# Kernel optimization log

Hardware: AMD Instinct MI355X
Metric: run time of the kernel (lower is better)

Reference implementation:

```python
import jax, jax.numpy as jnp
import numpy as np

EPS = 1e-5
K = 7            # involution kernel size
GC = 16          # group_channels (involution default)
RED = 4          # reduction ratio (involution default)


def _bn(x, g, b, m, v):
    # eval-mode BatchNorm2d over channel dim of NCHW
    scale = g / jnp.sqrt(v + EPS)
    return x * scale[None, :, None, None] + (b - m * scale)[None, :, None, None]


def setup_inputs() -> dict:
    key = jax.random.key(0)
    ks = jax.random.split(key, 24)
    C_in, C_out = 64, 128
    B, H, W = 4, 96, 96
    G = C_in // GC          # 4 involution groups
    Cr = C_in // RED        # 16 reduced channels

    def bn_params(k, c):
        k1, k2, k3, k4 = jax.random.split(k, 4)
        return (jax.random.uniform(k1, (c,)) + 0.5,          # gamma
                jax.random.normal(k2, (c,)) * 0.1,            # beta
                jax.random.normal(k3, (c,)) * 0.1,            # running mean
                jax.random.uniform(k4, (c,)) + 0.5)           # running var

    g_r, b_r, m_r, v_r = bn_params(ks[1], Cr)
    g_i, b_i, m_i, v_i = bn_params(ks[2], C_in)
    g_c, b_c, m_c, v_c = bn_params(ks[3], C_out)
    g_m, b_m, m_m, v_m = bn_params(ks[4], C_out)

    return {
        "x": jax.random.normal(ks[0], (B, C_in, H, W), dtype=jnp.float32),
        "w_reduce": jax.random.normal(ks[5], (Cr, C_in), dtype=jnp.float32) * 0.1,
        "g_r": g_r, "b_r": b_r, "m_r": m_r, "v_r": v_r,
        "w_span": jax.random.normal(ks[6], (K * K * G, Cr), dtype=jnp.float32) * 0.1,
        "b_span": jax.random.normal(ks[7], (K * K * G,), dtype=jnp.float32) * 0.1,
        "g_i": g_i, "b_i": b_i, "m_i": m_i, "v_i": v_i,
        "w_conv": jax.random.normal(ks[8], (C_out, C_in), dtype=jnp.float32) * 0.1,
        "g_c": g_c, "b_c": b_c, "m_c": m_c, "v_c": v_c,
        "w_map": jax.random.normal(ks[9], (C_out, C_in), dtype=jnp.float32) * 0.1,
        "b_map": jax.random.normal(ks[10], (C_out,), dtype=jnp.float32) * 0.1,
        "g_m": g_m, "b_m": b_m, "m_m": m_m, "v_m": v_m,
    }


def reference(x, w_reduce, g_r, b_r, m_r, v_r, w_span, b_span,
              g_i, b_i, m_i, v_i, w_conv, g_c, b_c, m_c, v_c,
              w_map, b_map, g_m, b_m, m_m, v_m):
    B, C, H, W = x.shape
    G = C // GC
    pad = (K - 1) // 2

    # --- Involution: dynamic per-pixel kernels ---
    t = jax.nn.relu(_bn(jnp.einsum('rc,bchw->brhw', w_reduce, x), g_r, b_r, m_r, v_r))
    kern = jnp.einsum('or,brhw->bohw', w_span, t) + b_span[None, :, None, None]
    kern = kern.reshape(B, G, 1, K * K, H, W)  # [B,G,1,KK,H,W]

    xp = jnp.pad(x, ((0, 0), (0, 0), (pad, pad), (pad, pad)))
    # unfold in torch (C, kh, kw) order: C slowest -> stack over kernel offsets
    patches = jnp.stack([xp[:, :, i:i + H, j:j + W]
                         for i in range(K) for j in range(K)], axis=2)  # [B,C,KK,H,W]
    patches = patches.reshape(B, G, GC, K * K, H, W)
    inv = (kern * patches).sum(axis=3).reshape(B, C, H, W)

    # --- BN + GELU, 1x1 conv + BN, mapping branch, residual + GELU ---
    x1 = jax.nn.gelu(_bn(inv, g_i, b_i, m_i, v_i), approximate=False)
    x1 = _bn(jnp.einsum('oc,bchw->bohw', w_conv, x1), g_c, b_c, m_c, v_c)
    xm = _bn(jnp.einsum('oc,bchw->bohw', w_map, x) + b_map[None, :, None, None],
             g_m, b_m, m_m, v_m)
    return jax.nn.gelu(x1 + xm, approximate=False)
```

## Files before the change

kernel.cpp:

```cpp
#include <hip/hip_runtime.h>
#include <hip/hip_bf16.h>
#include <math.h>

typedef __hip_bfloat16 bf16;
typedef __attribute__((ext_vector_type(8))) short v8s;
typedef __attribute__((ext_vector_type(4))) short v4s;
typedef __attribute__((ext_vector_type(4))) float v4f;

#define HD 96
#define WD 96
#define HW 9216
#define BATCH 4
#define NPIX (BATCH * HW)

#define OFF_WR    0
#define OFF_CR    1024
#define OFF_WSP   1040
#define OFF_BSP   4176
#define OFF_SI    4372
#define OFF_CI    4436
#define OFF_BIAS  4500
#define WFRAG_BYTE 18512
#define TG_BYTE   51328
#define ZT_BYTE   1230976
#define XBF_BYTE  10668160

__device__ __forceinline__ float geluf(float v) {
    return 0.5f * v * (1.0f + erff(v * 0.7071067811865475f));
}
__device__ __forceinline__ float upbf(short s) {
    unsigned int uu = ((unsigned int)(unsigned short)s) << 16;
    return __builtin_bit_cast(float, uu);
}
__device__ __forceinline__ v4f up4(v4s s) {
    v4f r;
    #pragma unroll
    for (int i = 0; i < 4; ++i) r[i] = upbf(s[i]);
    return r;
}
__device__ __forceinline__ short pkbf(float f) {
    return (short)__bfloat16_as_ushort(__float2bfloat16(f));
}

__global__ __launch_bounds__(256) void k_pre(
    const float* __restrict__ x,
    const float* __restrict__ wred,
    const float* __restrict__ gr, const float* __restrict__ br,
    const float* __restrict__ mr, const float* __restrict__ vr,
    const float* __restrict__ wspan, const float* __restrict__ bspan,
    const float* __restrict__ gi, const float* __restrict__ bi,
    const float* __restrict__ mi, const float* __restrict__ vi,
    const float* __restrict__ wconv,
    const float* __restrict__ gc, const float* __restrict__ bc,
    const float* __restrict__ mc, const float* __restrict__ vc,
    const float* __restrict__ wmap, const float* __restrict__ bmap,
    const float* __restrict__ gm, const float* __restrict__ bm,
    const float* __restrict__ mmn, const float* __restrict__ vm,
    float* __restrict__ wsf, bf16* __restrict__ wfrag,
    bf16* __restrict__ tg, v4s* __restrict__ xbf)
{
    const int tid = threadIdx.x;
    const int blk = blockIdx.x;

    if (blk < 64) {
        const int gt = blk * 256 + tid;
        if (gt < 1024) {
            int r = gt >> 6;
            float sr = gr[r] * rsqrtf(vr[r] + 1e-5f);
            wsf[OFF_WR + gt] = sr * wred[gt];
        }
        if (gt < 16) {
            float sr = gr[gt] * rsqrtf(vr[gt] + 1e-5f);
            wsf[OFF_CR + gt] = br[gt] - mr[gt] * sr;
        }
        if (gt < 3136) wsf[OFF_WSP + gt] = wspan[gt];
        if (gt < 196)  wsf[OFF_BSP + gt] = bspan[gt];
        if (gt < 64) {
            float si = gi[gt] * rsqrtf(vi[gt] + 1e-5f);
            wsf[OFF_SI + gt] = si;
            wsf[OFF_CI + gt] = bi[gt] - mi[gt] * si;
        }
        if (gt < 128) {
            float sc = gc[gt] * rsqrtf(vc[gt] + 1e-5f);
            float sm = gm[gt] * rsqrtf(vm[gt] + 1e-5f);
            wsf[OFF_BIAS + gt] = (bc[gt] - mc[gt] * sc)
                               + sm * bmap[gt]
                               + (bm[gt] - mmn[gt] * sm);
        }
        {
            int j    = gt & 7;
            int lane = (gt >> 3) & 63;
            int ks   = (gt >> 9) & 3;
            int mt   = gt >> 11;
            int m = mt * 16 + (lane & 15);
            int k = ks * 32 + (lane >> 4) * 8 + j;
            float v;
            if (k < 64) {
                float sc = gc[m] * rsqrtf(vc[m] + 1e-5f);
                v = sc * wconv[m * 64 + k];
            } else {
                float sm = gm[m] * rsqrtf(vm[m] + 1e-5f);
                v = sm * wmap[m * 64 + (k - 64)];
            }
            wfrag[gt] = __float2bfloat16(v);
        }
        return;
    }

    __shared__ float wrl[1024];
    __shared__ float crl[16];
    for (int i = tid; i < 1024; i += 256) {
        int r = i >> 6;
        wrl[i] = gr[r] * rsqrtf(vr[r] + 1e-5f) * wred[i];
    }
    if (tid < 16)
        crl[tid] = br[tid] - mr[tid] * gr[tid] * rsqrtf(vr[tid] + 1e-5f);
    __syncthreads();

    const int p = tid & 63, u = tid >> 6;
    const int gpix = (blk - 64) * 64 + p;
    const int b = gpix / HW, hw = gpix % HW;
    const float* xb = x + (size_t)b * 64 * HW + hw;
    v4s* xbf_b = xbf + (size_t)b * 16 * HW;

    float t4[4];
    #pragma unroll
    for (int r = 0; r < 4; ++r) t4[r] = crl[u * 4 + r];
    #pragma unroll 4
    for (int c4 = 0; c4 < 16; ++c4) {
        float xc0 = xb[(size_t)(c4 * 4 + 0) * HW];
        float xc1 = xb[(size_t)(c4 * 4 + 1) * HW];
        float xc2 = xb[(size_t)(c4 * 4 + 2) * HW];
        float xc3 = xb[(size_t)(c4 * 4 + 3) * HW];
        #pragma unroll
        for (int r = 0; r < 4; ++r) {
            v4f w = *(const v4f*)&wrl[(u * 4 + r) * 64 + c4 * 4];
            t4[r] += w[0] * xc0 + w[1] * xc1 + w[2] * xc2 + w[3] * xc3;
        }
        if ((c4 >> 2) == u) {
            v4s xv;
            xv[0] = pkbf(xc0); xv[1] = pkbf(xc1);
            xv[2] = pkbf(xc2); xv[3] = pkbf(xc3);
            xbf_b[(size_t)c4 * HW + hw] = xv;
        }
    }
    v4s pk;
    #pragma unroll
    for (int r = 0; r < 4; ++r) pk[r] = pkbf(fmaxf(t4[r], 0.0f));
    *(v4s*)((short*)tg + (size_t)gpix * 16 + u * 4) = pk;
}

__global__ __launch_bounds__(256) void k_inv3(
    const v4s* __restrict__ xbf, const float* __restrict__ wsf,
    const bf16* __restrict__ tg, bf16* __restrict__ zt)
{
    __shared__ v4s   xh[4 * 196];
    __shared__ float ksh[49 * 64];

    const int tid = threadIdx.x;
    const int bz  = blockIdx.z;
    const int b   = bz >> 2, g = bz & 3;
    const int ty  = blockIdx.y * 8, tx = blockIdx.x * 8;

    const v4s* xbf_b = xbf + (size_t)b * 16 * HW;

    for (int it = tid; it < 784; it += 256) {
        int qc = it / 196, pos = it % 196;
        int py = pos / 14, px = pos % 14;
        int gy = ty + py - 3, gx = tx + px - 3;
        v4s v = (v4s){0, 0, 0, 0};
        if (gy >= 0 && gy < HD && gx >= 0 && gx < WD)
            v = xbf_b[(size_t)(g * 4 + qc) * HW + gy * WD + gx];
        xh[it] = v;
    }

    const int p  = tid & 63;
    const int u  = __builtin_amdgcn_readfirstlane(tid >> 6);
    const int py0 = p >> 3, px0 = p & 7;
    const int hw  = (ty + py0) * WD + (tx + px0);
    const int gpix = b * HW + hw;

    const v8s* tp = (const v8s*)((const short*)tg + (size_t)gpix * 16);
    v8s t01 = tp[0], t23 = tp[1];
    float tr[16];
    #pragma unroll
    for (int i = 0; i < 8; ++i) { tr[i] = upbf(t01[i]); tr[8 + i] = upbf(t23[i]); }

    for (int kk = u; kk < 49; kk += 4) {
        int row = g * 49 + kk;
        float kv = wsf[OFF_BSP + row];
        #pragma unroll
        for (int r = 0; r < 16; ++r) kv += wsf[OFF_WSP + row * 16 + r] * tr[r];
        ksh[kk * 64 + p] = kv;
    }
    __syncthreads();

    float acc[4] = {0.f, 0.f, 0.f, 0.f};
    #pragma unroll 1
    for (int i = 0; i < 7; ++i) {
        const int rowb = (py0 + i) * 14 + px0;
        #pragma unroll
        for (int j = 0; j < 7; ++j) {
            float kv = ksh[(i * 7 + j) * 64 + p];
            v4f xv = up4(xh[u * 196 + rowb + j]);
            acc[0] += kv * xv[0];
            acc[1] += kv * xv[1];
            acc[2] += kv * xv[2];
            acc[3] += kv * xv[3];
        }
    }

    const int c0 = g * 16 + u * 4;
    bf16* ztr = zt + ((size_t)b * HW + hw) * 128;

    v4s pk1;
    #pragma unroll
    for (int ci = 0; ci < 4; ++ci) {
        float v = acc[ci] * wsf[OFF_SI + c0 + ci] + wsf[OFF_CI + c0 + ci];
        pk1[ci] = pkbf(geluf(v));
    }
    *(v4s*)&ztr[c0] = pk1;
    *(v4s*)&ztr[64 + c0] = xh[u * 196 + (py0 + 3) * 14 + (px0 + 3)];
}

__global__ __launch_bounds__(256) void k_out3(
    const bf16* __restrict__ zt, const float* __restrict__ wsf,
    const bf16* __restrict__ wfrag, float* __restrict__ out)
{
    const int tid  = threadIdx.x;
    const int lane = tid & 63;
    const int mq   = tid >> 6;
    const int n    = lane & 15;
    const int quad = lane >> 4;

    const int pxg = blockIdx.x * 16 + n;
    const int b   = pxg / HW;
    const int hw  = pxg % HW;

    const v8s* zb = (const v8s*)(zt + (size_t)pxg * 128);
    v8s bfr[4];
    #pragma unroll
    for (int ki = 0; ki < 4; ++ki) bfr[ki] = zb[ki * 4 + quad];

    const v8s* wf = (const v8s*)wfrag;
    v4f acc[2];
    acc[0] = (v4f){0.f, 0.f, 0.f, 0.f};
    acc[1] = (v4f){0.f, 0.f, 0.f, 0.f};

    #pragma unroll
    for (int ki = 0; ki < 4; ++ki) {
        #pragma unroll
        for (int m = 0; m < 2; ++m) {
            int mt = mq * 2 + m;
            v8s afrag = wf[(mt * 4 + ki) * 64 + lane];
            acc[m] = __builtin_amdgcn_mfma_f32_16x16x32_bf16(afrag, bfr[ki], acc[m], 0, 0, 0);
        }
    }

    #pragma unroll
    for (int m = 0; m < 2; ++m) {
        int m0 = (mq * 2 + m) * 16 + quad * 4;
        v4f bs = *(const v4f*)&wsf[OFF_BIAS + m0];
        #pragma unroll
        for (int reg = 0; reg < 4; ++reg) {
            float v = acc[m][reg] + bs[reg];
            out[((size_t)(b * 128 + m0 + reg)) * HW + hw] = geluf(v);
        }
    }
}

extern "C" void kernel_launch(void* const* d_in, const int* in_sizes, int n_in,
                              void* d_out, int out_size, void* d_ws, size_t ws_size,
                              hipStream_t stream)
{
    const float* x     = (const float*)d_in[0];
    const float* wred  = (const float*)d_in[1];
    const float* gr    = (const float*)d_in[2];
    const float* br    = (const float*)d_in[3];
    const float* mr    = (const float*)d_in[4];
    const float* vr    = (const float*)d_in[5];
    const float* wspan = (const float*)d_in[6];
    const float* bspan = (const float*)d_in[7];
    const float* gi    = (const float*)d_in[8];
    const float* bi    = (const float*)d_in[9];
    const float* mi    = (const float*)d_in[10];
    const float* vi    = (const float*)d_in[11];
    const float* wconv = (const float*)d_in[12];
    const float* gc    = (const float*)d_in[13];
    const float* bc    = (const float*)d_in[14];
    const float* mc    = (const float*)d_in[15];
    const float* vc    = (const float*)d_in[16];
    const float* wmap  = (const float*)d_in[17];
    const float* bmap  = (const float*)d_in[18];
    const float* gm    = (const float*)d_in[19];
    const float* bm    = (const float*)d_in[20];
    const float* mmn   = (const float*)d_in[21];
    const float* vm    = (const float*)d_in[22];

    float* wsf   = (float*)d_ws;
    bf16*  wfrag = (bf16*)((char*)d_ws + WFRAG_BYTE);
    bf16*  tg    = (bf16*)((char*)d_ws + TG_BYTE);
    bf16*  zt    = (bf16*)((char*)d_ws + ZT_BYTE);
    v4s*   xbf   = (v4s*)((char*)d_ws + XBF_BYTE);
    float* out   = (float*)d_out;

    hipLaunchKernelGGL(k_pre, dim3(64 + NPIX / 64), dim3(256), 0, stream,
                       x, wred, gr, br, mr, vr, wspan, bspan, gi, bi, mi, vi,
                       wconv, gc, bc, mc, vc, wmap, bmap, gm, bm, mmn, vm,
                       wsf, wfrag, tg, xbf);
    hipLaunchKernelGGL(k_inv3, dim3(12, 12, 16), dim3(256), 0, stream,
                       xbf, wsf, tg, zt);
    hipLaunchKernelGGL(k_out3, dim3(NPIX / 16), dim3(256), 0, stream,
                       zt, wsf, wfrag, out);
}
```

Baseline: 144.2 us.

## Halve intermediate buffer by reading x directly in output GEMM kernel

```diff
diff --git a/kernel.cpp b/kernel.cpp
--- a/kernel.cpp
+++ b/kernel.cpp
@@ -23,7 +23,7 @@
 #define WFRAG_BYTE 18512
 #define TG_BYTE   51328
 #define ZT_BYTE   1230976
-#define XBF_BYTE  10668160
+#define XBF_BYTE  5949568
 
 __device__ __forceinline__ float geluf(float v) {
     return 0.5f * v * (1.0f + erff(v * 0.7071067811865475f));
@@ -152,7 +152,7 @@
 
 __global__ __launch_bounds__(256) void k_inv3(
     const v4s* __restrict__ xbf, const float* __restrict__ wsf,
-    const bf16* __restrict__ tg, bf16* __restrict__ zt)
+    const bf16* __restrict__ tg, bf16* __restrict__ zt64)
 {
     __shared__ v4s   xh[4 * 196];
     __shared__ float ksh[49 * 64];
@@ -198,68 +198,80 @@
     float acc[4] = {0.f, 0.f, 0.f, 0.f};
     #pragma unroll 1
     for (int i = 0; i < 7; ++i) {
-        const int rowb = (py0 + i) * 14 + px0;
+        const int rowb = u * 196 + (py0 + i) * 14 + px0;
+        float kr[7];
+        #pragma unroll
+        for (int j = 0; j < 7; ++j) kr[j] = ksh[(i * 7 + j) * 64 + p];
         #pragma unroll
         for (int j = 0; j < 7; ++j) {
-            float kv = ksh[(i * 7 + j) * 64 + p];
-            v4f xv = up4(xh[u * 196 + rowb + j]);
-            acc[0] += kv * xv[0];
-            acc[1] += kv * xv[1];
-            acc[2] += kv * xv[2];
-            acc[3] += kv * xv[3];
+            v4f xv = up4(xh[rowb + j]);
+            acc[0] += kr[j] * xv[0];
+            acc[1] += kr[j] * xv[1];
+            acc[2] += kr[j] * xv[2];
+            acc[3] += kr[j] * xv[3];
         }
     }
 
     const int c0 = g * 16 + u * 4;
-    bf16* ztr = zt + ((size_t)b * HW + hw) * 128;
-
     v4s pk1;
     #pragma unroll
     for (int ci = 0; ci < 4; ++ci) {
         float v = acc[ci] * wsf[OFF_SI + c0 + ci] + wsf[OFF_CI + c0 + ci];
         pk1[ci] = pkbf(geluf(v));
     }
-    *(v4s*)&ztr[c0] = pk1;
-    *(v4s*)&ztr[64 + c0] = xh[u * 196 + (py0 + 3) * 14 + (px0 + 3)];
-}
-
-__global__ __launch_bounds__(256) void k_out3(
-    const bf16* __restrict__ zt, const float* __restrict__ wsf,
-    const bf16* __restrict__ wfrag, float* __restrict__ out)
+    *(v4s*)&zt64[(size_t)gpix * 64 + c0] = pk1;
+}
+
+__global__ __launch_bounds__(256) void k_out4(
+    const bf16* __restrict__ zt64, const v4s* __restrict__ xbf,
+    const float* __restrict__ wsf, const bf16* __restrict__ wfrag,
+    float* __restrict__ out)
 {
     const int tid  = threadIdx.x;
     const int lane = tid & 63;
-    const int mq   = tid >> 6;
+    const int wv   = tid >> 6;
+    const int pg   = wv >> 1;
+    const int mh   = wv & 1;
     const int n    = lane & 15;
     const int quad = lane >> 4;
 
-    const int pxg = blockIdx.x * 16 + n;
+    const int pxg = blockIdx.x * 32 + pg * 16 + n;
     const int b   = pxg / HW;
     const int hw  = pxg % HW;
 
-    const v8s* zb = (const v8s*)(zt + (size_t)pxg * 128);
+    const v8s* zb = (const v8s*)(zt64 + (size_t)pxg * 64);
     v8s bfr[4];
-    #pragma unroll
-    for (int ki = 0; ki < 4; ++ki) bfr[ki] = zb[ki * 4 + quad];
+    bfr[0] = zb[quad];
+    bfr[1] = zb[4 + quad];
+    const v4s* xq = xbf + (size_t)b * 16 * HW + hw;
+    #pragma unroll
+    for (int ks2 = 0; ks2 < 2; ++ks2) {
+        v4s a = xq[(size_t)(ks2 * 8 + 2 * quad) * HW];
+        v4s c = xq[(size_t)(ks2 * 8 + 2 * quad + 1) * HW];
+        v8s r;
+        #pragma unroll
+        for (int j = 0; j < 4; ++j) { r[j] = a[j]; r[4 + j] = c[j]; }
+        bfr[2 + ks2] = r;
+    }
 
     const v8s* wf = (const v8s*)wfrag;
-    v4f acc[2];
-    acc[0] = (v4f){0.f, 0.f, 0.f, 0.f};
-    acc[1] = (v4f){0.f, 0.f, 0.f, 0.f};
-
-    #pragma unroll
-    for (int ki = 0; ki < 4; ++ki) {
-        #pragma unroll
-        for (int m = 0; m < 2; ++m) {
-            int mt = mq * 2 + m;
-            v8s afrag = wf[(mt * 4 + ki) * 64 + lane];
-            acc[m] = __builtin_amdgcn_mfma_f32_16x16x32_bf16(afrag, bfr[ki], acc[m], 0, 0, 0);
-        }
-    }
-
-    #pragma unroll
-    for (int m = 0; m < 2; ++m) {
-        int m0 = (mq * 2 + m) * 16 + quad * 4;
+    v4f acc[4];
+    #pragma unroll
+    for (int m = 0; m < 4; ++m) acc[m] = (v4f){0.f, 0.f, 0.f, 0.f};
+
+    #pragma unroll
+    for (int ks = 0; ks < 4; ++ks) {
+        #pragma unroll
+        for (int m = 0; m < 4; ++m) {
+            int mt = mh * 4 + m;
+            v8s afrag = wf[(mt * 4 + ks) * 64 + lane];
+            acc[m] = __builtin_amdgcn_mfma_f32_16x16x32_bf16(afrag, bfr[ks], acc[m], 0, 0, 0);
+        }
+    }
+
+    #pragma unroll
+    for (int m = 0; m < 4; ++m) {
+        int m0 = (mh * 4 + m) * 16 + quad * 4;
         v4f bs = *(const v4f*)&wsf[OFF_BIAS + m0];
         #pragma unroll
         for (int reg = 0; reg < 4; ++reg) {
@@ -300,7 +312,7 @@
     float* wsf   = (float*)d_ws;
     bf16*  wfrag = (bf16*)((char*)d_ws + WFRAG_BYTE);
     bf16*  tg    = (bf16*)((char*)d_ws + TG_BYTE);
-    bf16*  zt    = (bf16*)((char*)d_ws + ZT_BYTE);
+    bf16*  zt64  = (bf16*)((char*)d_ws + ZT_BYTE);
     v4s*   xbf   = (v4s*)((char*)d_ws + XBF_BYTE);
     float* out   = (float*)d_out;
 
@@ -309,7 +321,7 @@
                        wconv, gc, bc, mc, vc, wmap, bmap, gm, bm, mmn, vm,
                        wsf, wfrag, tg, xbf);
     hipLaunchKernelGGL(k_inv3, dim3(12, 12, 16), dim3(256), 0, stream,
-                       xbf, wsf, tg, zt);
-    hipLaunchKernelGGL(k_out3, dim3(NPIX / 16), dim3(256), 0, stream,
-                       zt, wsf, wfrag, out);
-}
+                       xbf, wsf, tg, zt64);
+    hipLaunchKernelGGL(k_out4, dim3(NPIX / 32), dim3(256), 0, stream,
+                       zt64, xbf, wsf, wfrag, out);
+}
```

Result: no change. 144.3 us (median of 2 runs) (+0.1%).
